# Performance work log

Measured on AMD Instinct MI355X. Metric: run time of the kernel, lower is better.

## Reference

```python
import jax, jax.numpy as jnp
import numpy as np

N_NODES = 100000
N_EDGES = 1600000
D_IN = 128
D_HID = 128
D_OUT = 128


def setup_inputs() -> dict:
    key = jax.random.key(0)
    ks = jax.random.split(key, 12)
    x = jax.random.normal(ks[0], (N_NODES, D_IN), dtype=jnp.float32)
    edge_index = jax.random.randint(ks[1], (2, N_EDGES), 0, N_NODES, dtype=jnp.int64)
    s = 0.05
    # GraphConv layer l: out = agg @ w_rel + x @ w_root + b  (lin_rel has bias, lin_root does not)
    w_rel1 = jax.random.normal(ks[2], (D_IN, D_HID), dtype=jnp.float32) * s
    w_root1 = jax.random.normal(ks[3], (D_IN, D_HID), dtype=jnp.float32) * s
    b1 = jax.random.normal(ks[4], (D_HID,), dtype=jnp.float32) * s
    w_rel2 = jax.random.normal(ks[5], (D_HID, D_HID), dtype=jnp.float32) * s
    w_root2 = jax.random.normal(ks[6], (D_HID, D_HID), dtype=jnp.float32) * s
    b2 = jax.random.normal(ks[7], (D_HID,), dtype=jnp.float32) * s
    w_rel3 = jax.random.normal(ks[8], (D_HID, D_OUT), dtype=jnp.float32) * s
    w_root3 = jax.random.normal(ks[9], (D_HID, D_OUT), dtype=jnp.float32) * s
    b3 = jax.random.normal(ks[10], (D_OUT,), dtype=jnp.float32) * s
    return {"x": x, "edge_index": edge_index,
            "w_rel1": w_rel1, "w_root1": w_root1, "b1": b1,
            "w_rel2": w_rel2, "w_root2": w_root2, "b2": b2,
            "w_rel3": w_rel3, "w_root3": w_root3, "b3": b3}


def _graph_conv(h, src, dst, w_rel, w_root, b):
    # sum-aggregate neighbor features (message = x_j, flow src -> dst),
    # then linear; identical math to PyG GraphConv with aggr='add'.
    agg = jax.ops.segment_sum(h[src], dst, num_segments=h.shape[0])
    return agg @ w_rel + h @ w_root + b


def reference(x, edge_index, w_rel1, w_root1, b1, w_rel2, w_root2, b2, w_rel3, w_root3, b3):
    src, dst = edge_index[0], edge_index[1]
    h = jax.nn.relu(_graph_conv(x, src, dst, w_rel1, w_root1, b1))
    h = jax.nn.relu(_graph_conv(h, src, dst, w_rel2, w_root2, b2))
    out = _graph_conv(h, src, dst, w_rel3, w_root3, b3)
    return out
```

## Files before the change

### kernel.cpp

```cpp
#include <hip/hip_runtime.h>
#include <hip/hip_bf16.h>
#include <stdint.h>

typedef __hip_bfloat16 bf16;
typedef __hip_bfloat162 bf162;

typedef __attribute__((ext_vector_type(8))) short short8;
typedef __attribute__((ext_vector_type(4))) float floatx4;

#define BSH   8
#define BSZ   256
#define CHUNK 8192
#define NBMAX 512


__device__ __forceinline__ float2 load2f(const bf16* __restrict__ p) {
    const unsigned int u = *(const unsigned int*)p;
    return make_float2(__uint_as_float((u & 0xffffu) << 16),
                       __uint_as_float(u & 0xffff0000u));
}


__global__ __launch_bounds__(256)
void cvt_kernel(const float* __restrict__ x, bf16* __restrict__ y, int n4) {
    int i = blockIdx.x * 256 + threadIdx.x;
    if (i < n4) {
        float4 v = ((const float4*)x)[i];
        bf162 a, b;
        a.x = __float2bfloat16(v.x); a.y = __float2bfloat16(v.y);
        b.x = __float2bfloat16(v.z); b.y = __float2bfloat16(v.w);
        ((bf162*)y)[i * 2]     = a;
        ((bf162*)y)[i * 2 + 1] = b;
    }
}

__global__ __launch_bounds__(256)
void prep_w_kernel(const float* __restrict__ wrel, const float* __restrict__ wroot,
                   bf16* __restrict__ wsw) {
    int t = blockIdx.x * 256 + threadIdx.x;
    if (t >= 4096) return;
    const int lane = t & 63;
    const int ct   = (t >> 6) & 7;
    const int kt   = t >> 9;
    const int kbase = kt * 32 + (lane >> 4) * 8;
    const int n     = ct * 16 + (lane & 15);
    bf16* q = wsw + (size_t)t * 8;
#pragma unroll
    for (int j = 0; j < 8; ++j) {
        const int k = kbase + j;
        const float v = (k < 128) ? wrel[k * 128 + n] : wroot[(k - 128) * 128 + n];
        q[j] = __float2bfloat16(v);
    }
}


__global__ __launch_bounds__(256)
void bhist_kernel(const int* __restrict__ dst, int* __restrict__ T,
                  int E, int NB, int GB) {
    __shared__ int lh[NBMAX];
    const int b = blockIdx.x;
    for (int u = threadIdx.x; u < NB; u += 256) lh[u] = 0;
    __syncthreads();
    const int beg = b * CHUNK, end = min(beg + CHUNK, E);
    for (int e = beg + threadIdx.x; e < end; e += 256)
        atomicAdd(&lh[dst[e] >> BSH], 1);
    __syncthreads();
    for (int u = threadIdx.x; u < NB; u += 256)
        T[u * GB + b] = lh[u];
}


__global__ __launch_bounds__(256)
void scan1_kernel(const int* __restrict__ deg, int* __restrict__ rp,
                  int* __restrict__ bsum, int n) {
    __shared__ int s[256];
    const int tid = threadIdx.x;
    const int i = blockIdx.x * 256 + tid;
    const int d = (i < n) ? deg[i] : 0;
    s[tid] = d;
    __syncthreads();
    for (int off = 1; off < 256; off <<= 1) {
        int u = (tid >= off) ? s[tid - off] : 0;
        __syncthreads();
        s[tid] += u;
        __syncthreads();
    }
    if (i < n) rp[i] = s[tid] - d;
    if (tid == 255) bsum[blockIdx.x] = s[255];
}

__global__ __launch_bounds__(512)
void scan2_kernel(int* __restrict__ bsum, int G) {
    __shared__ int s[512];
    const int tid = threadIdx.x;
    const int d = (tid < G) ? bsum[tid] : 0;
    s[tid] = d;
    __syncthreads();
    for (int off = 1; off < 512; off <<= 1) {
        int u = (tid >= off) ? s[tid - off] : 0;
        __syncthreads();
        s[tid] += u;
        __syncthreads();
    }
    if (tid < G) bsum[tid] = s[tid] - d;
}

__global__ __launch_bounds__(256)
void scan3_kernel(int* __restrict__ rp, const int* __restrict__ bsum, int n) {
    const int i = blockIdx.x * 256 + threadIdx.x;
    if (i < n) rp[i] += bsum[blockIdx.x];
}


__global__ __launch_bounds__(256)
void bscatter_kernel(const int* __restrict__ src, const int* __restrict__ dst,
                     const int* __restrict__ T, int* __restrict__ ebuf,
                     int E, int NB, int GB) {
    __shared__ int lofs[NBMAX];
    const int b = blockIdx.x;
    for (int u = threadIdx.x; u < NB; u += 256)
        lofs[u] = T[u * GB + b];
    __syncthreads();
    const int beg = b * CHUNK, end = min(beg + CHUNK, E);
    for (int e = beg + threadIdx.x; e < end; e += 256) {
        const int d = dst[e];
        const int u = d >> BSH;
        const int pos = atomicAdd(&lofs[u], 1);
        ebuf[pos] = (src[e] << BSH) | (d & (BSZ - 1));
    }
}


__global__ __launch_bounds__(256)
void bbuild_kernel(const int* __restrict__ T, const int* __restrict__ ebuf,
                   int* __restrict__ rp, int* __restrict__ col,
                   int E, int N, int NB, int GB) {
    __shared__ int s[256];
    __shared__ int lrank[256];
    const int u = blockIdx.x;
    const int tid = threadIdx.x;
    const int beg = T[u * GB];
    const int end = (u + 1 < NB) ? T[(u + 1) * GB] : E;

    lrank[tid] = 0;
    __syncthreads();
    for (int e = beg + tid; e < end; e += 256)
        atomicAdd(&lrank[ebuf[e] & (BSZ - 1)], 1);
    __syncthreads();
    const int cntv = lrank[tid];
    s[tid] = cntv;
    __syncthreads();
    for (int off = 1; off < 256; off <<= 1) {
        int v = (tid >= off) ? s[tid - off] : 0;
        __syncthreads();
        s[tid] += v;
        __syncthreads();
    }
    const int excl = s[tid] - cntv;
    const int node = u * BSZ + tid;
    if (node < N) rp[node] = beg + excl;
    if (u == NB - 1 && tid == 0) rp[N] = E;
    lrank[tid] = beg + excl;
    __syncthreads();
    for (int e = beg + tid; e < end; e += 256) {
        const int p = ebuf[e];
        const int pos = atomicAdd(&lrank[p & (BSZ - 1)], 1);
        col[pos] = p >> BSH;
    }
}


__global__ __launch_bounds__(256)
void agg_kernel(const bf16* __restrict__ h, const int* __restrict__ rp,
                const int* __restrict__ col, bf16* __restrict__ agg, int N) {
    const int lane = threadIdx.x & 63;
    const int wid  = threadIdx.x >> 6;
    const int node = blockIdx.x * 4 + wid;
    if (node >= N) return;
    const int beg = rp[node], end = rp[node + 1];
    const int f = lane * 2;
    float2 acc = make_float2(0.f, 0.f);
    int e = beg;
    for (; e + 4 <= end; e += 4) {
        const int s0 = col[e], s1 = col[e + 1], s2 = col[e + 2], s3 = col[e + 3];
        const float2 a = load2f(h + (size_t)s0 * 128 + f);
        const float2 b = load2f(h + (size_t)s1 * 128 + f);
        const float2 c = load2f(h + (size_t)s2 * 128 + f);
        const float2 d = load2f(h + (size_t)s3 * 128 + f);
        acc.x += (a.x + b.x) + (c.x + d.x);
        acc.y += (a.y + b.y) + (c.y + d.y);
    }
    for (; e < end; ++e) {
        const int s0 = col[e];
        const float2 a = load2f(h + (size_t)s0 * 128 + f);
        acc.x += a.x;
        acc.y += a.y;
    }
    bf162 o;
    o.x = __float2bfloat16(acc.x);
    o.y = __float2bfloat16(acc.y);
    *(bf162*)(agg + (size_t)node * 128 + f) = o;
}


template <bool RELU, typename OT>
__global__ __launch_bounds__(256)
void mfma_gemm_kernel(const bf16* __restrict__ Aagg, const bf16* __restrict__ Hroot,
                      const bf16* __restrict__ wsw, const float* __restrict__ bias,
                      OT* __restrict__ out, int M) {
    const int tid  = threadIdx.x;
    const int lane = tid & 63;
    const int wave = tid >> 6;
    const int l15  = lane & 15;
    const int quad = lane >> 4;

    const int row_a = blockIdx.x * 64 + wave * 16 + l15;
    const bool rowok = row_a < M;

    floatx4 acc[8];
#pragma unroll
    for (int ct = 0; ct < 8; ++ct) acc[ct] = (floatx4){0.f, 0.f, 0.f, 0.f};

#pragma unroll
    for (int kt = 0; kt < 8; ++kt) {
        const bf16* Abase = (kt < 4) ? Aagg : Hroot;
        const int k0 = (kt & 3) * 32 + quad * 8;
        short8 afrag = (short8){0, 0, 0, 0, 0, 0, 0, 0};
        if (rowok) afrag = *(const short8*)(Abase + (size_t)row_a * 128 + k0);
#pragma unroll
        for (int ct = 0; ct < 8; ++ct) {
            const short8 bfrag = *(const short8*)(wsw + (size_t)((kt * 8 + ct) * 64 + lane) * 8);
            acc[ct] = __builtin_amdgcn_mfma_f32_16x16x32_bf16(afrag, bfrag, acc[ct], 0, 0, 0);
        }
    }

    const int row_o = blockIdx.x * 64 + wave * 16 + quad * 4;
#pragma unroll
    for (int ct = 0; ct < 8; ++ct) {
        const int colc = ct * 16 + l15;
        const float bv = bias[colc];
#pragma unroll
        for (int r = 0; r < 4; ++r) {
            const int row = row_o + r;
            if (row < M) {
                float v = acc[ct][r] + bv;
                if (RELU) v = fmaxf(v, 0.f);
                if constexpr (sizeof(OT) == 2)
                    ((bf16*)out)[(size_t)row * 128 + colc] = __float2bfloat16(v);
                else
                    ((float*)out)[(size_t)row * 128 + colc] = v;
            }
        }
    }
}


extern "C" void kernel_launch(void* const* d_in, const int* in_sizes, int n_in,
                              void* d_out, int out_size, void* d_ws, size_t ws_size,
                              hipStream_t stream) {
    const float* x       = (const float*)d_in[0];
    const int*   ei      = (const int*)d_in[1];
    const float* w_rel1  = (const float*)d_in[2];
    const float* w_root1 = (const float*)d_in[3];
    const float* b1      = (const float*)d_in[4];
    const float* w_rel2  = (const float*)d_in[5];
    const float* w_root2 = (const float*)d_in[6];
    const float* b2      = (const float*)d_in[7];
    const float* w_rel3  = (const float*)d_in[8];
    const float* w_root3 = (const float*)d_in[9];
    const float* b3      = (const float*)d_in[10];
    float* out = (float*)d_out;

    const int N = in_sizes[0] / 128;
    const int E = in_sizes[1] / 2;
    const int* src = ei;
    const int* dst = ei + E;

    char* w = (char*)d_ws;
    auto alloc = [&](size_t bytes) {
        char* p = w;
        w += (bytes + 255) & ~(size_t)255;
        return p;
    };
    int*  col  = (int*)alloc((size_t)E * 4);
    int*  rp   = (int*)alloc((size_t)(N + 1) * 4);
    bf16* h1   = (bf16*)alloc((size_t)N * 128 * 2);
    bf16* xbf  = (bf16*)alloc((size_t)N * 128 * 2);
    bf16* agg  = (bf16*)alloc((size_t)N * 128 * 2);
    bf16* wsw1 = (bf16*)alloc(32768 * 2);
    bf16* wsw2 = (bf16*)alloc(32768 * 2);
    bf16* wsw3 = (bf16*)alloc(32768 * 2);
    bf16* h2   = xbf;
    int*  T    = (int*)h1;
    int*  bsum = (int*)(h1 + 1024 * 1024);
    int*  ebuf = (int*)agg;

    const int NB = (N + BSZ - 1) / BSZ;
    const int GB = (E + CHUNK - 1) / CHUNK;
    const int nT = NB * GB;
    const int scanTBlocks = (nT + 255) / 256;

    const int aggBlocks  = (N + 3) / 4;
    const int gemmBlocks = (N + 63) / 64;
    const int cvtBlocks  = (N * 32 + 255) / 256;

    cvt_kernel<<<cvtBlocks, 256, 0, stream>>>(x, xbf, N * 32);
    prep_w_kernel<<<16, 256, 0, stream>>>(w_rel1, w_root1, wsw1);
    prep_w_kernel<<<16, 256, 0, stream>>>(w_rel2, w_root2, wsw2);
    prep_w_kernel<<<16, 256, 0, stream>>>(w_rel3, w_root3, wsw3);

    bhist_kernel<<<GB, 256, 0, stream>>>(dst, T, E, NB, GB);
    scan1_kernel<<<scanTBlocks, 256, 0, stream>>>(T, T, bsum, nT);
    scan2_kernel<<<1, 512, 0, stream>>>(bsum, scanTBlocks);
    scan3_kernel<<<scanTBlocks, 256, 0, stream>>>(T, bsum, nT);
    bscatter_kernel<<<GB, 256, 0, stream>>>(src, dst, T, ebuf, E, NB, GB);
    bbuild_kernel<<<NB, 256, 0, stream>>>(T, ebuf, rp, col, E, N, NB, GB);

    agg_kernel<<<aggBlocks, 256, 0, stream>>>(xbf, rp, col, agg, N);
    mfma_gemm_kernel<true, bf16><<<gemmBlocks, 256, 0, stream>>>(agg, xbf, wsw1, b1, h1, N);
    agg_kernel<<<aggBlocks, 256, 0, stream>>>(h1, rp, col, agg, N);
    mfma_gemm_kernel<true, bf16><<<gemmBlocks, 256, 0, stream>>>(agg, h1, wsw2, b2, h2, N);
    agg_kernel<<<aggBlocks, 256, 0, stream>>>(h2, rp, col, agg, N);
    mfma_gemm_kernel<false, float><<<gemmBlocks, 256, 0, stream>>>(agg, h2, wsw3, b3, out, N);
}
```

Baseline: 505.2 us.

## Fuse neighbor aggregation into GEMM kernel via LDS staging

```diff
diff --git a/kernel.cpp b/kernel.cpp
--- a/kernel.cpp
+++ b/kernel.cpp
@@ -12,6 +12,7 @@
 #define BSZ   256
 #define CHUNK 8192
 #define NBMAX 512
+#define ASTRIDE 136
 
 
 __device__ __forceinline__ float2 load2f(const bf16* __restrict__ p) {
@@ -69,7 +70,6 @@
         T[u * GB + b] = lh[u];
 }
 
-
 __global__ __launch_bounds__(256)
 void scan1_kernel(const int* __restrict__ deg, int* __restrict__ rp,
                   int* __restrict__ bsum, int n) {
@@ -111,7 +111,6 @@
     if (i < n) rp[i] += bsum[blockIdx.x];
 }
 
-
 __global__ __launch_bounds__(256)
 void bscatter_kernel(const int* __restrict__ src, const int* __restrict__ dst,
                      const int* __restrict__ T, int* __restrict__ ebuf,
@@ -129,7 +128,6 @@
         ebuf[pos] = (src[e] << BSH) | (d & (BSZ - 1));
     }
 }
-
 
 __global__ __launch_bounds__(256)
 void bbuild_kernel(const int* __restrict__ T, const int* __restrict__ ebuf,
@@ -170,52 +168,69 @@
 }
 
 
-__global__ __launch_bounds__(256)
-void agg_kernel(const bf16* __restrict__ h, const int* __restrict__ rp,
-                const int* __restrict__ col, bf16* __restrict__ agg, int N) {
-    const int lane = threadIdx.x & 63;
-    const int wid  = threadIdx.x >> 6;
-    const int node = blockIdx.x * 4 + wid;
-    if (node >= N) return;
-    const int beg = rp[node], end = rp[node + 1];
-    const int f = lane * 2;
-    float2 acc = make_float2(0.f, 0.f);
-    int e = beg;
-    for (; e + 4 <= end; e += 4) {
-        const int s0 = col[e], s1 = col[e + 1], s2 = col[e + 2], s3 = col[e + 3];
-        const float2 a = load2f(h + (size_t)s0 * 128 + f);
-        const float2 b = load2f(h + (size_t)s1 * 128 + f);
-        const float2 c = load2f(h + (size_t)s2 * 128 + f);
-        const float2 d = load2f(h + (size_t)s3 * 128 + f);
-        acc.x += (a.x + b.x) + (c.x + d.x);
-        acc.y += (a.y + b.y) + (c.y + d.y);
-    }
-    for (; e < end; ++e) {
-        const int s0 = col[e];
-        const float2 a = load2f(h + (size_t)s0 * 128 + f);
-        acc.x += a.x;
-        acc.y += a.y;
-    }
-    bf162 o;
-    o.x = __float2bfloat16(acc.x);
-    o.y = __float2bfloat16(acc.y);
-    *(bf162*)(agg + (size_t)node * 128 + f) = o;
-}
-
-
 template <bool RELU, typename OT>
 __global__ __launch_bounds__(256)
-void mfma_gemm_kernel(const bf16* __restrict__ Aagg, const bf16* __restrict__ Hroot,
-                      const bf16* __restrict__ wsw, const float* __restrict__ bias,
-                      OT* __restrict__ out, int M) {
+void fused_layer_kernel(const bf16* __restrict__ h, const int* __restrict__ rp,
+                        const int* __restrict__ col, const bf16* __restrict__ wsw,
+                        const float* __restrict__ bias, OT* __restrict__ out, int N) {
+    __shared__ bf16 As[64 * ASTRIDE];
     const int tid  = threadIdx.x;
     const int lane = tid & 63;
     const int wave = tid >> 6;
     const int l15  = lane & 15;
     const int quad = lane >> 4;
-
-    const int row_a = blockIdx.x * 64 + wave * 16 + l15;
-    const bool rowok = row_a < M;
+    const int node0 = blockIdx.x * 64;
+
+    const int row_a = node0 + wave * 16 + l15;
+    const bool rowok = row_a < N;
+    short8 rootfrag[4];
+#pragma unroll
+    for (int kt = 0; kt < 4; ++kt) {
+        rootfrag[kt] = (short8){0, 0, 0, 0, 0, 0, 0, 0};
+        if (rowok)
+            rootfrag[kt] = *(const short8*)(h + (size_t)row_a * 128 + kt * 32 + quad * 8);
+    }
+
+    const int f = lane * 2;
+    for (int i = 0; i < 16; ++i) {
+        const int node = node0 + wave * 16 + i;
+        float2 acc = make_float2(0.f, 0.f);
+        if (node < N) {
+            const int beg = rp[node], endd = rp[node + 1];
+            int e = beg;
+            for (; e + 8 <= endd; e += 8) {
+                const int s0 = col[e],     s1 = col[e + 1], s2 = col[e + 2], s3 = col[e + 3];
+                const int s4 = col[e + 4], s5 = col[e + 5], s6 = col[e + 6], s7 = col[e + 7];
+                const float2 a0 = load2f(h + (size_t)s0 * 128 + f);
+                const float2 a1 = load2f(h + (size_t)s1 * 128 + f);
+                const float2 a2 = load2f(h + (size_t)s2 * 128 + f);
+                const float2 a3 = load2f(h + (size_t)s3 * 128 + f);
+                const float2 a4 = load2f(h + (size_t)s4 * 128 + f);
+                const float2 a5 = load2f(h + (size_t)s5 * 128 + f);
+                const float2 a6 = load2f(h + (size_t)s6 * 128 + f);
+                const float2 a7 = load2f(h + (size_t)s7 * 128 + f);
+                acc.x += ((a0.x + a1.x) + (a2.x + a3.x)) + ((a4.x + a5.x) + (a6.x + a7.x));
+                acc.y += ((a0.y + a1.y) + (a2.y + a3.y)) + ((a4.y + a5.y) + (a6.y + a7.y));
+            }
+            for (; e + 2 <= endd; e += 2) {
+                const int s0 = col[e], s1 = col[e + 1];
+                const float2 a0 = load2f(h + (size_t)s0 * 128 + f);
+                const float2 a1 = load2f(h + (size_t)s1 * 128 + f);
+                acc.x += a0.x + a1.x;
+                acc.y += a0.y + a1.y;
+            }
+            if (e < endd) {
+                const float2 a0 = load2f(h + (size_t)col[e] * 128 + f);
+                acc.x += a0.x;
+                acc.y += a0.y;
+            }
+        }
+        bf162 o;
+        o.x = __float2bfloat16(acc.x);
+        o.y = __float2bfloat16(acc.y);
+        *(bf162*)(As + (wave * 16 + i) * ASTRIDE + f) = o;
+    }
+    __syncthreads();
 
     floatx4 acc[8];
 #pragma unroll
@@ -223,10 +238,11 @@
 
 #pragma unroll
     for (int kt = 0; kt < 8; ++kt) {
-        const bf16* Abase = (kt < 4) ? Aagg : Hroot;
-        const int k0 = (kt & 3) * 32 + quad * 8;
-        short8 afrag = (short8){0, 0, 0, 0, 0, 0, 0, 0};
-        if (rowok) afrag = *(const short8*)(Abase + (size_t)row_a * 128 + k0);
+        short8 afrag;
+        if (kt < 4)
+            afrag = *(const short8*)(As + (wave * 16 + l15) * ASTRIDE + kt * 32 + quad * 8);
+        else
+            afrag = rootfrag[kt - 4];
 #pragma unroll
         for (int ct = 0; ct < 8; ++ct) {
             const short8 bfrag = *(const short8*)(wsw + (size_t)((kt * 8 + ct) * 64 + lane) * 8);
@@ -234,7 +250,7 @@
         }
     }
 
-    const int row_o = blockIdx.x * 64 + wave * 16 + quad * 4;
+    const int row_o = node0 + wave * 16 + quad * 4;
 #pragma unroll
     for (int ct = 0; ct < 8; ++ct) {
         const int colc = ct * 16 + l15;
@@ -242,7 +258,7 @@
 #pragma unroll
         for (int r = 0; r < 4; ++r) {
             const int row = row_o + r;
-            if (row < M) {
+            if (row < N) {
                 float v = acc[ct][r] + bv;
                 if (RELU) v = fmaxf(v, 0.f);
                 if constexpr (sizeof(OT) == 2)
@@ -284,25 +300,23 @@
     };
     int*  col  = (int*)alloc((size_t)E * 4);
     int*  rp   = (int*)alloc((size_t)(N + 1) * 4);
+    int*  ebuf = (int*)alloc((size_t)E * 4);
     bf16* h1   = (bf16*)alloc((size_t)N * 128 * 2);
     bf16* xbf  = (bf16*)alloc((size_t)N * 128 * 2);
-    bf16* agg  = (bf16*)alloc((size_t)N * 128 * 2);
     bf16* wsw1 = (bf16*)alloc(32768 * 2);
     bf16* wsw2 = (bf16*)alloc(32768 * 2);
     bf16* wsw3 = (bf16*)alloc(32768 * 2);
     bf16* h2   = xbf;
     int*  T    = (int*)h1;
     int*  bsum = (int*)(h1 + 1024 * 1024);
-    int*  ebuf = (int*)agg;
 
     const int NB = (N + BSZ - 1) / BSZ;
     const int GB = (E + CHUNK - 1) / CHUNK;
     const int nT = NB * GB;
     const int scanTBlocks = (nT + 255) / 256;
 
-    const int aggBlocks  = (N + 3) / 4;
-    const int gemmBlocks = (N + 63) / 64;
-    const int cvtBlocks  = (N * 32 + 255) / 256;
+    const int layerBlocks = (N + 63) / 64;
+    const int cvtBlocks   = (N * 32 + 255) / 256;
 
     cvt_kernel<<<cvtBlocks, 256, 0, stream>>>(x, xbf, N * 32);
     prep_w_kernel<<<16, 256, 0, stream>>>(w_rel1, w_root1, wsw1);
@@ -316,10 +330,7 @@
     bscatter_kernel<<<GB, 256, 0, stream>>>(src, dst, T, ebuf, E, NB, GB);
     bbuild_kernel<<<NB, 256, 0, stream>>>(T, ebuf, rp, col, E, N, NB, GB);
 
-    agg_kernel<<<aggBlocks, 256, 0, stream>>>(xbf, rp, col, agg, N);
-    mfma_gemm_kernel<true, bf16><<<gemmBlocks, 256, 0, stream>>>(agg, xbf, wsw1, b1, h1, N);
-    agg_kernel<<<aggBlocks, 256, 0, stream>>>(h1, rp, col, agg, N);
-    mfma_gemm_kernel<true, bf16><<<gemmBlocks, 256, 0, stream>>>(agg, h1, wsw2, b2, h2, N);
-    agg_kernel<<<aggBlocks, 256, 0, stream>>>(h2, rp, col, agg, N);
-    mfma_gemm_kernel<false, float><<<gemmBlocks, 256, 0, stream>>>(agg, h2, wsw3, b3, out, N);
-}
+    fused_layer_kernel<true, bf16><<<layerBlocks, 256, 0, stream>>>(xbf, rp, col, wsw1, b1, h1, N);
+    fused_layer_kernel<true, bf16><<<layerBlocks, 256, 0, stream>>>(h1, rp, col, wsw2, b2, h2, N);
+    fused_layer_kernel<false, float><<<layerBlocks, 256, 0, stream>>>(h2, rp, col, wsw3, b3, out, N);
+}
```

Measured after the change: 571.6 us. +13.2%, slower.
